# Kernel tuning notes

Hardware: AMD Instinct MI355X
Metric: run time of the kernel (lower is better)

Reference implementation:

```python
import jax, jax.numpy as jnp
import numpy as np

N = 50000   # total nodes across batched graphs
E = 800000  # total edges
F = 30      # input node features
G = 256     # number of graphs in the disjoint batch
CH = [128, 64, 32]
N_LABELS = 2


def setup_inputs() -> dict:
    key = jax.random.key(0)
    ks = jax.random.split(key, 16)
    x = jax.random.normal(ks[0], (N, F), dtype=jnp.float32)
    edge_weight = jax.random.uniform(ks[1], (E,), dtype=jnp.float32)
    edge_row = jax.random.randint(ks[2], (E,), 0, N, dtype=jnp.int32)
    edge_col = jax.random.randint(ks[3], (E,), 0, N, dtype=jnp.int32)
    seg = jnp.sort(jax.random.randint(ks[4], (N,), 0, G, dtype=jnp.int32))
    # GCSConv params: out = A @ (x W1) + x W2 + b, per layer
    dims = [F] + CH
    params = {}
    kk = 5
    for l in range(3):
        fin, fout = dims[l], dims[l + 1]
        s = 1.0 / np.sqrt(fin)
        params[f"w1_{l+1}"] = jax.random.uniform(ks[kk], (fin, fout), minval=-s, maxval=s, dtype=jnp.float32); kk += 1
        params[f"w2_{l+1}"] = jax.random.uniform(ks[kk], (fin, fout), minval=-s, maxval=s, dtype=jnp.float32); kk += 1
        params[f"b_{l+1}"] = jnp.zeros((fout,), dtype=jnp.float32)
    sd = 1.0 / np.sqrt(CH[-1])
    params["wd"] = jax.random.uniform(ks[kk], (CH[-1], N_LABELS), minval=-sd, maxval=sd, dtype=jnp.float32)
    params["bd"] = jnp.zeros((N_LABELS,), dtype=jnp.float32)
    return {"x": x, "edge_weight": edge_weight, "edge_row": edge_row,
            "edge_col": edge_col, "seg": seg, **params}


def _gcs_conv(x, ew, er, ec, w1, w2, b):
    # spektral GCSConv: relu(A @ (x W1) + x W2 + b) with sparse A in COO form
    h = x @ w1                                   # [N, Fout]
    msgs = ew[:, None] * h[ec]                   # gather along edges [E, Fout]
    agg = jax.ops.segment_sum(msgs, er, num_segments=N)  # SpMM scatter [N, Fout]
    return jax.nn.relu(agg + x @ w2 + b)


def reference(x, edge_weight, edge_row, edge_col, seg,
              w1_1, w2_1, b_1, w1_2, w2_2, b_2, w1_3, w2_3, b_3, wd, bd):
    h = _gcs_conv(x, edge_weight, edge_row, edge_col, w1_1, w2_1, b_1)
    h = _gcs_conv(h, edge_weight, edge_row, edge_col, w1_2, w2_2, b_2)
    h = _gcs_conv(h, edge_weight, edge_row, edge_col, w1_3, w2_3, b_3)
    # GlobalAvgPool: segment mean over graph ids
    sums = jax.ops.segment_sum(h, seg, num_segments=G)               # [G, 32]
    cnts = jax.ops.segment_sum(jnp.ones((N,), h.dtype), seg, num_segments=G)
    pooled = sums / jnp.maximum(cnts, 1.0)[:, None]
    return jax.nn.softmax(pooled @ wd + bd, axis=-1)                 # [G, 2]
```

## Files before the change

### kernel.cpp

```cpp
#include <hip/hip_runtime.h>
#include <hip/hip_fp16.h>

#define N_NODES 50000
#define N_EDGES 800000
#define N_GRAPHS 256
#define NCB 196
#define CHUNK 3125
#define MBLK 782

typedef _Float16 f16x8 __attribute__((ext_vector_type(8)));
typedef float    f32x4 __attribute__((ext_vector_type(4)));

__global__ __launch_bounds__(256)
void hist_prep(const int* __restrict__ ER, const float* __restrict__ X,
               const int* __restrict__ SEG,
               const float* __restrict__ W1, const float* __restrict__ W2,
               const float* __restrict__ W12, const float* __restrict__ W22,
               const float* __restrict__ W13, const float* __restrict__ W23,
               int* __restrict__ ghist, __half* __restrict__ XPh,
               int* __restrict__ start,
               __half* __restrict__ W1f, __half* __restrict__ W2f,
               __half* __restrict__ W3f, float* __restrict__ PS)
{
    int b = blockIdx.x;
    int t = threadIdx.x;
    if (b < 256) {
        __shared__ int h[NCB];
        for (int i = t; i < NCB; i += 256) h[i] = 0;
        __syncthreads();
        int lo = b * CHUNK, hi = lo + CHUNK;
        for (int e = lo + t; e < hi; e += 256) atomicAdd(&h[ER[e] >> 8], 1);
        __syncthreads();
        for (int i = t; i < NCB; i += 256) ghist[i * 256 + b] = h[i];
        return;
    }
    int bid = b - 256;
    if (bid < 6250) {
        int idx = bid * 256 + t;
        int n = idx >> 5;
        int c = idx & 31;
        float v = (c < 30) ? X[n * 30 + c] : 0.f;
        XPh[(size_t)n * 32 + c] = __float2half(v);
    } else if (bid < 6446) {
        int n = (bid - 6250) * 256 + t;
        if (n >= N_NODES) return;
        int g = SEG[n];
        int gprev = (n == 0) ? -1 : SEG[n - 1];
        for (int gg = gprev + 1; gg <= g; ++gg) start[gg] = n;
        if (n == N_NODES - 1)
            for (int gg = g + 1; gg <= N_GRAPHS; ++gg) start[gg] = N_NODES;
    } else if (bid < 6558) {
        int idx = (bid - 6446) * 256 + t;
        if (idx < 8192) {
            int i = idx & 7, c = (idx >> 3) & 15, g = (idx >> 7) & 3;
            int s = (idx >> 9) & 1, n = idx >> 10;
            int k = s * 32 + g * 8 + i, col = n * 16 + c;
            float w = 0.f;
            if (k < 30) w = W1[k * 128 + col];
            else if (k >= 32 && k < 62) w = W2[(k - 32) * 128 + col];
            W1f[idx] = __float2half(w);
        } else if (idx < 24576) {
            int o = idx - 8192;
            int i = o & 7, c = (o >> 3) & 15, g = (o >> 7) & 3;
            int s = (o >> 9) & 3, n = o >> 11;
            int k = s * 32 + g * 8 + i, col = n * 16 + c;
            float w = (col < 64) ? W12[k * 64 + col] : W22[k * 64 + col - 64];
            W2f[o] = __float2half(w);
        } else {
            int o = idx - 24576;
            int i = o & 7, c = (o >> 3) & 15, g = (o >> 7) & 3;
            int s = (o >> 9) & 1, n = o >> 10;
            int k = s * 32 + g * 8 + i, col = n * 16 + c;
            float w = (col < 32) ? W13[k * 32 + col] : W23[k * 32 + col - 32];
            W3f[o] = __float2half(w);
        }
    } else {
        int idx = (bid - 6558) * 256 + t;
        PS[idx] = 0.f;
    }
}

__global__ __launch_bounds__(256)
void scan1(int* __restrict__ ghist, int* __restrict__ bsum)
{
    __shared__ int s[256];
    int t = threadIdx.x, b = blockIdx.x;
    int i = b * 256 + t;
    int v = ghist[i];
    s[t] = v;
    __syncthreads();
    for (int off = 1; off < 256; off <<= 1) {
        int u = (t >= off) ? s[t - off] : 0;
        __syncthreads();
        s[t] += u;
        __syncthreads();
    }
    ghist[i] = s[t] - v;
    if (t == 255) bsum[b] = s[255];
}

__global__ __launch_bounds__(256)
void c_scatter(const int* __restrict__ ER, const int* __restrict__ EC,
               const float* __restrict__ EW, const int* __restrict__ ghist,
               const int* __restrict__ bsum, unsigned int* __restrict__ tmp_sd,
               __half* __restrict__ tmp_w)
{
    __shared__ int s[256];
    __shared__ int cur[NCB];
    int t = threadIdx.x, blk = blockIdx.x;
    int v = (t < NCB) ? bsum[t] : 0;
    s[t] = v;
    __syncthreads();
    for (int off = 1; off < 256; off <<= 1) {
        int u = (t >= off) ? s[t - off] : 0;
        __syncthreads();
        s[t] += u;
        __syncthreads();
    }
    if (t < NCB) cur[t] = (s[t] - v) + ghist[t * 256 + blk];
    __syncthreads();
    int lo = blk * CHUNK, hi = lo + CHUNK;
    for (int e = lo + t; e < hi; e += 256) {
        int d = ER[e];
        int pos = atomicAdd(&cur[d >> 8], 1);
        tmp_sd[pos] = (unsigned int)EC[e] | ((unsigned int)(d & 255) << 16);
        tmp_w[pos] = __float2half(EW[e]);
    }
}

__device__ __forceinline__ void fma8h(float4& a0, float4& a1, float w,
                                      const uint4& raw)
{
    const __half2* hp = (const __half2*)&raw;
    float2 f0 = __half22float2(hp[0]);
    float2 f1 = __half22float2(hp[1]);
    float2 f2 = __half22float2(hp[2]);
    float2 f3 = __half22float2(hp[3]);
    a0.x = fmaf(w, f0.x, a0.x); a0.y = fmaf(w, f0.y, a0.y);
    a0.z = fmaf(w, f1.x, a0.z); a0.w = fmaf(w, f1.y, a0.w);
    a1.x = fmaf(w, f2.x, a1.x); a1.y = fmaf(w, f2.y, a1.y);
    a1.z = fmaf(w, f3.x, a1.z); a1.w = fmaf(w, f3.y, a1.w);
}

__global__ __launch_bounds__(512)
void bsort_aggx(const unsigned int* __restrict__ tmp_sd, const __half* __restrict__ tmp_w,
                const int* __restrict__ bsum, const __half* __restrict__ XPh,
                unsigned int* __restrict__ packed, int* __restrict__ rowptr,
                __half* __restrict__ CIa)
{
    __shared__ int s[256];
    __shared__ int hist[256];
    __shared__ int cur[256];
    __shared__ int r0arr[257];
    int t = threadIdx.x, b = blockIdx.x;

    if (t < 256) s[t] = (t < NCB) ? bsum[t] : 0;
    __syncthreads();
    for (int off = 1; off < 256; off <<= 1) {
        int u = 0;
        if (t < 256 && t >= off) u = s[t - off];
        __syncthreads();
        if (t < 256) s[t] += u;
        __syncthreads();
    }
    int cntb = bsum[b];
    int base = s[b] - cntb;
    int end  = base + cntb;
    __syncthreads();

    if (t < 256) hist[t] = 0;
    __syncthreads();
    for (int j = base + t; j < end; j += 512)
        atomicAdd(&hist[(tmp_sd[j] >> 16) & 255], 1);
    __syncthreads();
    int hv = 0;
    if (t < 256) { hv = hist[t]; s[t] = hv; }
    __syncthreads();
    for (int off = 1; off < 256; off <<= 1) {
        int u = 0;
        if (t < 256 && t >= off) u = s[t - off];
        __syncthreads();
        if (t < 256) s[t] += u;
        __syncthreads();
    }
    if (t < 256) {
        int excl = s[t] - hv;
        int n = b * 256 + t;
        if (n < N_NODES) rowptr[n] = base + excl;
        if (b == NCB - 1 && t == 0) rowptr[N_NODES] = N_EDGES;
        r0arr[t] = base + excl;
        cur[t] = base + excl;
        if (t == 0) r0arr[256] = end;
    }
    __syncthreads();
    for (int j = base + t; j < end; j += 512) {
        unsigned int sd = tmp_sd[j];
        unsigned short hb = __half_as_ushort(tmp_w[j]);
        int pos = atomicAdd(&cur[(sd >> 16) & 255], 1);
        packed[pos] = (sd & 0xFFFF) | ((unsigned int)hb << 16);
    }
    __syncthreads();

    #pragma unroll
    for (int pass = 0; pass < 2; ++pass) {
        int local = pass * 128 + (t >> 2);
        int q = t & 3;
        int n = b * 256 + local;
        if (n < N_NODES) {
            int r0 = r0arr[local], r1 = r0arr[local + 1];
            float4 acc0 = make_float4(0.f, 0.f, 0.f, 0.f);
            float4 acc1 = make_float4(0.f, 0.f, 0.f, 0.f);
            int j = r0;
            for (; j + 3 < r1; j += 4) {
                unsigned int ra = packed[j],     rb = packed[j + 1];
                unsigned int rc = packed[j + 2], rd = packed[j + 3];
                uint4 rawa = *(const uint4*)(XPh + (size_t)(ra & 0xFFFF) * 32 + q * 8);
                uint4 rawb = *(const uint4*)(XPh + (size_t)(rb & 0xFFFF) * 32 + q * 8);
                uint4 rawc = *(const uint4*)(XPh + (size_t)(rc & 0xFFFF) * 32 + q * 8);
                uint4 rawd = *(const uint4*)(XPh + (size_t)(rd & 0xFFFF) * 32 + q * 8);
                float wa = __half2float(__ushort_as_half((unsigned short)(ra >> 16)));
                float wb = __half2float(__ushort_as_half((unsigned short)(rb >> 16)));
                float wc = __half2float(__ushort_as_half((unsigned short)(rc >> 16)));
                float wd = __half2float(__ushort_as_half((unsigned short)(rd >> 16)));
                fma8h(acc0, acc1, wa, rawa);
                fma8h(acc0, acc1, wb, rawb);
                fma8h(acc0, acc1, wc, rawc);
                fma8h(acc0, acc1, wd, rawd);
            }
            for (; j < r1; ++j) {
                unsigned int r = packed[j];
                uint4 raw = *(const uint4*)(XPh + (size_t)(r & 0xFFFF) * 32 + q * 8);
                float w = __half2float(__ushort_as_half((unsigned short)(r >> 16)));
                fma8h(acc0, acc1, w, raw);
            }
            __half2 hb2[4];
            hb2[0] = __float22half2_rn(make_float2(acc0.x, acc0.y));
            hb2[1] = __float22half2_rn(make_float2(acc0.z, acc0.w));
            hb2[2] = __float22half2_rn(make_float2(acc1.x, acc1.y));
            hb2[3] = __float22half2_rn(make_float2(acc1.z, acc1.w));
            *(uint4*)(CIa + (size_t)n * 32 + q * 8) = *(uint4*)&hb2[0];
        }
    }
}

__global__ __launch_bounds__(256)
void dense12_mfma(const __half* __restrict__ CIa, const __half* __restrict__ XPh,
                  const __half* __restrict__ W1f, const float* __restrict__ B1,
                  const __half* __restrict__ W2f, const float* __restrict__ B2,
                  __half* __restrict__ H2h, __half* __restrict__ A2h)
{
    __shared__ __align__(16) __half As[64 * 72];
    __shared__ __align__(16) __half Hs[64 * 136];
    const int tid = threadIdx.x;
    const int m0 = blockIdx.x * 64;
    const int lane = tid & 63;
    const int w  = tid >> 6;
    const int lr = lane & 15;
    const int lg = lane >> 4;

    for (int idx = tid; idx < 512; idx += 256) {
        int row = idx >> 3, c8 = idx & 7;
        int gm = m0 + row;
        uint4 v = make_uint4(0, 0, 0, 0);
        if (gm < N_NODES) {
            const __half* src = (c8 < 4) ? (CIa + (size_t)gm * 32 + c8 * 8)
                                         : (XPh + (size_t)gm * 32 + (c8 - 4) * 8);
            v = *(const uint4*)src;
        }
        *(uint4*)(As + row * 72 + c8 * 8) = v;
    }
    __syncthreads();

    f32x4 acc[4][2];
    #pragma unroll
    for (int m = 0; m < 4; ++m)
        #pragma unroll
        for (int j = 0; j < 2; ++j)
            acc[m][j] = (f32x4){0.f, 0.f, 0.f, 0.f};

    #pragma unroll
    for (int s = 0; s < 2; ++s) {
        f16x8 a[4];
        #pragma unroll
        for (int m = 0; m < 4; ++m)
            a[m] = *(const f16x8*)(As + (m * 16 + lr) * 72 + s * 32 + lg * 8);
        #pragma unroll
        for (int j = 0; j < 2; ++j) {
            const int n = 2 * w + j;
            f16x8 b = *(const f16x8*)(W1f + (((n * 2 + s) * 4 + lg) * 16 + lr) * 8);
            #pragma unroll
            for (int m = 0; m < 4; ++m)
                acc[m][j] = __builtin_amdgcn_mfma_f32_16x16x32_f16(a[m], b, acc[m][j], 0, 0, 0);
        }
    }

    #pragma unroll
    for (int j = 0; j < 2; ++j) {
        const int n = 2 * w + j;
        const float bias = B1[n * 16 + lr];
        #pragma unroll
        for (int m = 0; m < 4; ++m)
            #pragma unroll
            for (int r = 0; r < 4; ++r) {
                float v = fmaxf(acc[m][j][r] + bias, 0.f);
                Hs[(m * 16 + lg * 4 + r) * 136 + n * 16 + lr] = __float2half(v);
            }
    }
    __syncthreads();

    f32x4 acc2[4][2];
    #pragma unroll
    for (int m = 0; m < 4; ++m)
        #pragma unroll
        for (int j = 0; j < 2; ++j)
            acc2[m][j] = (f32x4){0.f, 0.f, 0.f, 0.f};

    #pragma unroll
    for (int s = 0; s < 4; ++s) {
        f16x8 a[4];
        #pragma unroll
        for (int m = 0; m < 4; ++m)
            a[m] = *(const f16x8*)(Hs + (m * 16 + lr) * 136 + s * 32 + lg * 8);
        #pragma unroll
        for (int j = 0; j < 2; ++j) {
            const int n = 2 * w + j;
            f16x8 b = *(const f16x8*)(W2f + (((n * 4 + s) * 4 + lg) * 16 + lr) * 8);
            #pragma unroll
            for (int m = 0; m < 4; ++m)
                acc2[m][j] = __builtin_amdgcn_mfma_f32_16x16x32_f16(a[m], b, acc2[m][j], 0, 0, 0);
        }
    }
    __syncthreads();

    #pragma unroll
    for (int j = 0; j < 2; ++j) {
        const int n = 2 * w + j;
        const float bias = (n >= 4) ? B2[(n - 4) * 16 + lr] : 0.f;
        #pragma unroll
        for (int m = 0; m < 4; ++m)
            #pragma unroll
            for (int r = 0; r < 4; ++r)
                Hs[(m * 16 + lg * 4 + r) * 136 + n * 16 + lr] =
                    __float2half(acc2[m][j][r] + bias);
    }
    __syncthreads();

    for (int idx = tid; idx < 1024; idx += 256) {
        int row = idx >> 4, c8 = idx & 15;
        int gm = m0 + row;
        if (gm < N_NODES) {
            uint4 v = *(const uint4*)(Hs + row * 136 + c8 * 8);
            if (c8 < 8) *(uint4*)(H2h + (size_t)gm * 64 + c8 * 8) = v;
            else        *(uint4*)(A2h + (size_t)gm * 64 + (c8 - 8) * 8) = v;
        }
    }
}

__global__ __launch_bounds__(512)
void spmm_dense3(const __half* __restrict__ H2h, const int* __restrict__ rowptr,
                 const unsigned int* __restrict__ packed,
                 const __half* __restrict__ A2h, const __half* __restrict__ W3f,
                 const float* __restrict__ B3, __half* __restrict__ H3h,
                 __half* __restrict__ B2h)
{
    __shared__ __align__(16) __half As[64 * 72];
    __shared__ __align__(16) __half Os[64 * 72];
    const int tid = threadIdx.x;
    const int m0 = blockIdx.x * 64;

    {
        int local = tid >> 3;
        int q = tid & 7;
        int n = m0 + local;
        float4 acc0 = make_float4(0.f, 0.f, 0.f, 0.f);
        float4 acc1 = make_float4(0.f, 0.f, 0.f, 0.f);
        if (n < N_NODES) {
            {
                uint4 raw = *(const uint4*)(A2h + (size_t)n * 64 + q * 8);
                const __half2* hp = (const __half2*)&raw;
                float2 f0 = __half22float2(hp[0]);
                float2 f1 = __half22float2(hp[1]);
                float2 f2 = __half22float2(hp[2]);
                float2 f3 = __half22float2(hp[3]);
                acc0 = make_float4(f0.x, f0.y, f1.x, f1.y);
                acc1 = make_float4(f2.x, f2.y, f3.x, f3.y);
            }
            int r0 = rowptr[n], r1 = rowptr[n + 1];
            int j = r0;
            for (; j + 3 < r1; j += 4) {
                unsigned int ra = packed[j],     rb = packed[j + 1];
                unsigned int rc = packed[j + 2], rd = packed[j + 3];
                uint4 rawa = *(const uint4*)(H2h + (size_t)(ra & 0xFFFF) * 64 + q * 8);
                uint4 rawb = *(const uint4*)(H2h + (size_t)(rb & 0xFFFF) * 64 + q * 8);
                uint4 rawc = *(const uint4*)(H2h + (size_t)(rc & 0xFFFF) * 64 + q * 8);
                uint4 rawd = *(const uint4*)(H2h + (size_t)(rd & 0xFFFF) * 64 + q * 8);
                float wa = __half2float(__ushort_as_half((unsigned short)(ra >> 16)));
                float wb = __half2float(__ushort_as_half((unsigned short)(rb >> 16)));
                float wc = __half2float(__ushort_as_half((unsigned short)(rc >> 16)));
                float wd = __half2float(__ushort_as_half((unsigned short)(rd >> 16)));
                fma8h(acc0, acc1, wa, rawa);
                fma8h(acc0, acc1, wb, rawb);
                fma8h(acc0, acc1, wc, rawc);
                fma8h(acc0, acc1, wd, rawd);
            }
            for (; j < r1; ++j) {
                unsigned int r = packed[j];
                uint4 raw = *(const uint4*)(H2h + (size_t)(r & 0xFFFF) * 64 + q * 8);
                float w = __half2float(__ushort_as_half((unsigned short)(r >> 16)));
                fma8h(acc0, acc1, w, raw);
            }
        }
        __half2 hb[4];
        hb[0] = __float22half2_rn(make_float2(fmaxf(acc0.x, 0.f), fmaxf(acc0.y, 0.f)));
        hb[1] = __float22half2_rn(make_float2(fmaxf(acc0.z, 0.f), fmaxf(acc0.w, 0.f)));
        hb[2] = __float22half2_rn(make_float2(fmaxf(acc1.x, 0.f), fmaxf(acc1.y, 0.f)));
        hb[3] = __float22half2_rn(make_float2(fmaxf(acc1.z, 0.f), fmaxf(acc1.w, 0.f)));
        *(uint4*)(As + local * 72 + q * 8) = *(uint4*)&hb[0];
    }
    __syncthreads();

    const int lane = tid & 63;
    const int w  = tid >> 6;
    const int wm = w >> 2;
    const int wn = w & 3;
    const int lr = lane & 15;
    const int lg = lane >> 4;

    f32x4 acc[2];
    acc[0] = (f32x4){0.f, 0.f, 0.f, 0.f};
    acc[1] = (f32x4){0.f, 0.f, 0.f, 0.f};

    #pragma unroll
    for (int s = 0; s < 2; ++s) {
        f16x8 b = *(const f16x8*)(W3f + (((wn * 2 + s) * 4 + lg) * 16 + lr) * 8);
        #pragma unroll
        for (int m = 0; m < 2; ++m) {
            int mm = wm * 2 + m;
            f16x8 a = *(const f16x8*)(As + (mm * 16 + lr) * 72 + s * 32 + lg * 8);
            acc[m] = __builtin_amdgcn_mfma_f32_16x16x32_f16(a, b, acc[m], 0, 0, 0);
        }
    }

    const float bias = (wn >= 2) ? B3[(wn - 2) * 16 + lr] : 0.f;
    #pragma unroll
    for (int m = 0; m < 2; ++m) {
        int mm = wm * 2 + m;
        #pragma unroll
        for (int r = 0; r < 4; ++r)
            Os[(mm * 16 + lg * 4 + r) * 72 + wn * 16 + lr] =
                __float2half(acc[m][r] + bias);
    }
    __syncthreads();

    {
        int row = tid >> 3, c8 = tid & 7;
        int gm = m0 + row;
        if (gm < N_NODES) {
            uint4 v = *(const uint4*)(Os + row * 72 + c8 * 8);
            if (c8 < 4) *(uint4*)(H3h + (size_t)gm * 32 + c8 * 8) = v;
            else        *(uint4*)(B2h + (size_t)gm * 32 + (c8 - 4) * 8) = v;
        }
    }
}

__global__ __launch_bounds__(256)
void spmm_pool(const __half* __restrict__ H, const int* __restrict__ rowptr,
               const unsigned int* __restrict__ packed,
               const __half* __restrict__ Bse, const int* __restrict__ SEG,
               float* __restrict__ PS)
{
    __shared__ float ps[65][32];
    int tid = threadIdx.x;
    int local = tid >> 2;
    int q = tid & 3;
    int n0 = blockIdx.x * 64;
    int n = n0 + local;
    for (int i = tid; i < 65 * 32; i += 256) ((float*)ps)[i] = 0.f;
    __syncthreads();
    int g0 = SEG[n0];
    if (n < N_NODES) {
        int g = SEG[n];
        int r0 = rowptr[n], r1 = rowptr[n + 1];
        float4 acc0, acc1;
        {
            uint4 raw = *(const uint4*)(Bse + (size_t)n * 32 + q * 8);
            const __half2* hp = (const __half2*)&raw;
            float2 f0 = __half22float2(hp[0]);
            float2 f1 = __half22float2(hp[1]);
            float2 f2 = __half22float2(hp[2]);
            float2 f3 = __half22float2(hp[3]);
            acc0 = make_float4(f0.x, f0.y, f1.x, f1.y);
            acc1 = make_float4(f2.x, f2.y, f3.x, f3.y);
        }
        int j = r0;
        for (; j + 3 < r1; j += 4) {
            unsigned int ra = packed[j],     rb = packed[j + 1];
            unsigned int rc = packed[j + 2], rd = packed[j + 3];
            uint4 rawa = *(const uint4*)(H + (size_t)(ra & 0xFFFF) * 32 + q * 8);
            uint4 rawb = *(const uint4*)(H + (size_t)(rb & 0xFFFF) * 32 + q * 8);
            uint4 rawc = *(const uint4*)(H + (size_t)(rc & 0xFFFF) * 32 + q * 8);
            uint4 rawd = *(const uint4*)(H + (size_t)(rd & 0xFFFF) * 32 + q * 8);
            float wa = __half2float(__ushort_as_half((unsigned short)(ra >> 16)));
            float wb = __half2float(__ushort_as_half((unsigned short)(rb >> 16)));
            float wc = __half2float(__ushort_as_half((unsigned short)(rc >> 16)));
            float wd = __half2float(__ushort_as_half((unsigned short)(rd >> 16)));
            fma8h(acc0, acc1, wa, rawa);
            fma8h(acc0, acc1, wb, rawb);
            fma8h(acc0, acc1, wc, rawc);
            fma8h(acc0, acc1, wd, rawd);
        }
        for (; j < r1; ++j) {
            unsigned int r = packed[j];
            uint4 raw = *(const uint4*)(H + (size_t)(r & 0xFFFF) * 32 + q * 8);
            float w = __half2float(__ushort_as_half((unsigned short)(r >> 16)));
            fma8h(acc0, acc1, w, raw);
        }
        float* dst = &ps[g - g0][q * 8];
        atomicAdd(&dst[0], fmaxf(acc0.x, 0.f));
        atomicAdd(&dst[1], fmaxf(acc0.y, 0.f));
        atomicAdd(&dst[2], fmaxf(acc0.z, 0.f));
        atomicAdd(&dst[3], fmaxf(acc0.w, 0.f));
        atomicAdd(&dst[4], fmaxf(acc1.x, 0.f));
        atomicAdd(&dst[5], fmaxf(acc1.y, 0.f));
        atomicAdd(&dst[6], fmaxf(acc1.z, 0.f));
        atomicAdd(&dst[7], fmaxf(acc1.w, 0.f));
    }
    __syncthreads();
    int nlast = n0 + 63;
    if (nlast >= N_NODES) nlast = N_NODES - 1;
    int span = SEG[nlast] - g0 + 1;
    for (int i = tid; i < span * 32; i += 256) {
        float v = ps[i >> 5][i & 31];
        if (v != 0.f)
            atomicAdd(&PS[(size_t)(g0 + (i >> 5)) * 32 + (i & 31)], v);
    }
}

__global__ __launch_bounds__(256)
void head_kernel(const float* __restrict__ PS, const int* __restrict__ start,
                 const float* __restrict__ WD, const float* __restrict__ BD,
                 float* __restrict__ OUT)
{
    int g = threadIdx.x;
    int s = start[g], e = start[g + 1];
    float inv = (e > s) ? 1.0f / (float)(e - s) : 1.0f;
    float l0 = 0.f, l1 = 0.f;
    #pragma unroll
    for (int j = 0; j < 32; ++j) {
        float p = PS[g * 32 + j] * inv;
        l0 = fmaf(p, WD[j * 2 + 0], l0);
        l1 = fmaf(p, WD[j * 2 + 1], l1);
    }
    l0 += BD[0]; l1 += BD[1];
    float m = fmaxf(l0, l1);
    float e0 = expf(l0 - m), e1 = expf(l1 - m);
    float si = 1.0f / (e0 + e1);
    OUT[g * 2 + 0] = e0 * si;
    OUT[g * 2 + 1] = e1 * si;
}

extern "C" void kernel_launch(void* const* d_in, const int* in_sizes, int n_in,
                              void* d_out, int out_size, void* d_ws, size_t ws_size,
                              hipStream_t stream)
{
    const float* x    = (const float*)d_in[0];
    const float* ew   = (const float*)d_in[1];
    const int*   er   = (const int*)d_in[2];
    const int*   ec   = (const int*)d_in[3];
    const int*   seg  = (const int*)d_in[4];
    const float* w1_1 = (const float*)d_in[5];
    const float* w2_1 = (const float*)d_in[6];
    const float* b_1  = (const float*)d_in[7];
    const float* w1_2 = (const float*)d_in[8];
    const float* w2_2 = (const float*)d_in[9];
    const float* b_2  = (const float*)d_in[10];
    const float* w1_3 = (const float*)d_in[11];
    const float* w2_3 = (const float*)d_in[12];
    const float* b_3  = (const float*)d_in[13];
    const float* wd   = (const float*)d_in[14];
    const float* bd   = (const float*)d_in[15];

    float* ws = (float*)d_ws;
    int*   IW = (int*)d_ws;
    __half* XPh    = (__half*)ws;
    __half* CIa    = (__half*)(ws + 800000);
    unsigned int* tmp_sd = (unsigned int*)(ws + 1600000);
    __half* tmp_w  = (__half*)(ws + 2400000);
    __half* H2h    = (__half*)(ws + 3200000);
    __half* A2h    = (__half*)(ws + 4800000);
    __half* H3h    = (__half*)(ws + 6400000);
    __half* B2h    = (__half*)(ws + 7200000);
    unsigned int* packed = (unsigned int*)(IW + 8000000);
    int*    rowptr = IW + 9000000;
    int*    ghist  = IW + 9060000;
    int*    bsum   = IW + 9115000;
    int*    start  = IW + 9120000;
    __half* W1f    = (__half*)(ws + 9125000);
    __half* W2f    = (__half*)(ws + 9130000);
    __half* W3f    = (__half*)(ws + 9139000);
    float*  PS     = ws + 9145000;

    dim3 blk(256);

    hist_prep<<<dim3(256 + 6590), blk, 0, stream>>>(er, x, seg, w1_1, w2_1,
                                                    w1_2, w2_2, w1_3, w2_3,
                                                    ghist, XPh, start,
                                                    W1f, W2f, W3f, PS);
    scan1<<<dim3(NCB), blk, 0, stream>>>(ghist, bsum);
    c_scatter<<<dim3(256), blk, 0, stream>>>(er, ec, ew, ghist, bsum, tmp_sd, tmp_w);
    bsort_aggx<<<dim3(NCB), dim3(512), 0, stream>>>(tmp_sd, tmp_w, bsum, XPh,
                                                    packed, rowptr, CIa);

    dense12_mfma<<<dim3(MBLK), blk, 0, stream>>>(CIa, XPh, W1f, b_1,
                                                 W2f, b_2, H2h, A2h);
    spmm_dense3<<<dim3(MBLK), dim3(512), 0, stream>>>(H2h, rowptr, packed, A2h,
                                                      W3f, b_3, H3h, B2h);
    spmm_pool<<<dim3(MBLK), blk, 0, stream>>>(H3h, rowptr, packed, B2h, seg, PS);
    head_kernel<<<dim3(1), blk, 0, stream>>>(PS, start, wd, bd, (float*)d_out);
}
```

Baseline: 182.4 us.

## Degree-sort nodes for SpMM load balancing across waves

Builds a global degree histogram and a permutation that orders nodes by in-degree, so the SpMM phases in spmm_dense3 and spmm_pool process rows of similar length together and warp divergence from uneven edge counts drops. bsort_aggx also reorders its local rows by degree. Because permuted rows no longer map to contiguous graphs, spmm_pool now keeps a full 256-graph shared accumulator and flushes all of it with global atomics. The cost is an extra kernel launch, gathers through the permutation that scatter the output writes, and a larger shared-memory pool with more atomic flushes.

```diff
diff --git a/kernel.cpp b/kernel.cpp
--- a/kernel.cpp
+++ b/kernel.cpp
@@ -20,7 +20,8 @@
                int* __restrict__ ghist, __half* __restrict__ XPh,
                int* __restrict__ start,
                __half* __restrict__ W1f, __half* __restrict__ W2f,
-               __half* __restrict__ W3f, float* __restrict__ PS)
+               __half* __restrict__ W3f, float* __restrict__ PS,
+               int* __restrict__ dhist, int* __restrict__ dcnt)
 {
     int b = blockIdx.x;
     int t = threadIdx.x;
@@ -76,7 +77,9 @@
         }
     } else {
         int idx = (bid - 6558) * 256 + t;
-        PS[idx] = 0.f;
+        if (idx < 8192) PS[idx] = 0.f;
+        else if (idx < 8256) dhist[idx - 8192] = 0;
+        else if (idx < 8320) dcnt[idx - 8256] = 0;
     }
 }
 
@@ -146,15 +149,19 @@
 void bsort_aggx(const unsigned int* __restrict__ tmp_sd, const __half* __restrict__ tmp_w,
                 const int* __restrict__ bsum, const __half* __restrict__ XPh,
                 unsigned int* __restrict__ packed, int* __restrict__ rowptr,
-                __half* __restrict__ CIa)
+                __half* __restrict__ CIa, int* __restrict__ dhist)
 {
     __shared__ int s[256];
     __shared__ int hist[256];
     __shared__ int cur[256];
     __shared__ int r0arr[257];
+    __shared__ int lh[64];
+    __shared__ int lbase[64];
+    __shared__ int lperm[256];
     int t = threadIdx.x, b = blockIdx.x;
 
     if (t < 256) s[t] = (t < NCB) ? bsum[t] : 0;
+    if (t >= 448) lh[t - 448] = 0;
     __syncthreads();
     for (int off = 1; off < 256; off <<= 1) {
         int u = 0;
@@ -183,6 +190,8 @@
         if (t < 256) s[t] += u;
         __syncthreads();
     }
+    int myd = 0, myrank = 0;
+    const int nvalid = (b * 256 + 256 <= N_NODES) ? 256 : (N_NODES - b * 256);
     if (t < 256) {
         int excl = s[t] - hv;
         int n = b * 256 + t;
@@ -191,8 +200,17 @@
         r0arr[t] = base + excl;
         cur[t] = base + excl;
         if (t == 0) r0arr[256] = end;
-    }
-    __syncthreads();
+        if (t < nvalid) {
+            myd = (hv < 63) ? hv : 63;
+            myrank = atomicAdd(&lh[myd], 1);
+        }
+    }
+    __syncthreads();
+    if (t < 64 && lh[t] > 0) atomicAdd(&dhist[t], lh[t]);
+    if (t == 511) {
+        int acc = 0;
+        for (int i = 0; i < 64; ++i) { lbase[i] = acc; acc += lh[i]; }
+    }
     for (int j = base + t; j < end; j += 512) {
         unsigned int sd = tmp_sd[j];
         unsigned short hb = __half_as_ushort(tmp_w[j]);
@@ -200,13 +218,16 @@
         packed[pos] = (sd & 0xFFFF) | ((unsigned int)hb << 16);
     }
     __syncthreads();
+    if (t < nvalid) lperm[lbase[myd] + myrank] = t;
+    __syncthreads();
 
     #pragma unroll
     for (int pass = 0; pass < 2; ++pass) {
-        int local = pass * 128 + (t >> 2);
+        int idx = pass * 128 + (t >> 2);
         int q = t & 3;
-        int n = b * 256 + local;
-        if (n < N_NODES) {
+        if (idx < nvalid) {
+            int local = lperm[idx];
+            int n = b * 256 + local;
             int r0 = r0arr[local], r1 = r0arr[local + 1];
             float4 acc0 = make_float4(0.f, 0.f, 0.f, 0.f);
             float4 acc1 = make_float4(0.f, 0.f, 0.f, 0.f);
@@ -244,6 +265,32 @@
 }
 
 __global__ __launch_bounds__(256)
+void perm_scatter(const int* __restrict__ rowptr, const int* __restrict__ dhist,
+                  int* __restrict__ dcnt, int* __restrict__ perm)
+{
+    __shared__ int lh[64], gbase[64], dbase[64];
+    int t = threadIdx.x, b = blockIdx.x;
+    int n = b * 256 + t;
+    if (t < 64) lh[t] = 0;
+    __syncthreads();
+    int d = 0, myr = 0;
+    bool valid = (n < N_NODES);
+    if (valid) {
+        d = rowptr[n + 1] - rowptr[n];
+        if (d > 63) d = 63;
+        myr = atomicAdd(&lh[d], 1);
+    }
+    __syncthreads();
+    if (t < 64) gbase[t] = (lh[t] > 0) ? atomicAdd(&dcnt[t], lh[t]) : 0;
+    if (t == 0) {
+        int acc = 0;
+        for (int i = 0; i < 64; ++i) { dbase[i] = acc; acc += dhist[i]; }
+    }
+    __syncthreads();
+    if (valid) perm[dbase[d] + gbase[d] + myr] = n;
+}
+
+__global__ __launch_bounds__(256)
 void dense12_mfma(const __half* __restrict__ CIa, const __half* __restrict__ XPh,
                   const __half* __restrict__ W1f, const float* __restrict__ B1,
                   const __half* __restrict__ W2f, const float* __restrict__ B2,
@@ -361,7 +408,7 @@
                  const unsigned int* __restrict__ packed,
                  const __half* __restrict__ A2h, const __half* __restrict__ W3f,
                  const float* __restrict__ B3, __half* __restrict__ H3h,
-                 __half* __restrict__ B2h)
+                 __half* __restrict__ B2h, const int* __restrict__ perm)
 {
     __shared__ __align__(16) __half As[64 * 72];
     __shared__ __align__(16) __half Os[64 * 72];
@@ -371,10 +418,11 @@
     {
         int local = tid >> 3;
         int q = tid & 7;
-        int n = m0 + local;
+        int i = m0 + local;
         float4 acc0 = make_float4(0.f, 0.f, 0.f, 0.f);
         float4 acc1 = make_float4(0.f, 0.f, 0.f, 0.f);
-        if (n < N_NODES) {
+        if (i < N_NODES) {
+            int n = perm[i];
             {
                 uint4 raw = *(const uint4*)(A2h + (size_t)n * 64 + q * 8);
                 const __half2* hp = (const __half2*)&raw;
@@ -454,8 +502,9 @@
 
     {
         int row = tid >> 3, c8 = tid & 7;
-        int gm = m0 + row;
-        if (gm < N_NODES) {
+        int i = m0 + row;
+        if (i < N_NODES) {
+            int gm = perm[i];
             uint4 v = *(const uint4*)(Os + row * 72 + c8 * 8);
             if (c8 < 4) *(uint4*)(H3h + (size_t)gm * 32 + c8 * 8) = v;
             else        *(uint4*)(B2h + (size_t)gm * 32 + (c8 - 4) * 8) = v;
@@ -467,18 +516,17 @@
 void spmm_pool(const __half* __restrict__ H, const int* __restrict__ rowptr,
                const unsigned int* __restrict__ packed,
                const __half* __restrict__ Bse, const int* __restrict__ SEG,
-               float* __restrict__ PS)
-{
-    __shared__ float ps[65][32];
+               float* __restrict__ PS, const int* __restrict__ perm)
+{
+    __shared__ float ps[N_GRAPHS][32];
     int tid = threadIdx.x;
     int local = tid >> 2;
     int q = tid & 3;
-    int n0 = blockIdx.x * 64;
-    int n = n0 + local;
-    for (int i = tid; i < 65 * 32; i += 256) ((float*)ps)[i] = 0.f;
-    __syncthreads();
-    int g0 = SEG[n0];
-    if (n < N_NODES) {
+    int i = blockIdx.x * 64 + local;
+    for (int k = tid; k < N_GRAPHS * 32; k += 256) ((float*)ps)[k] = 0.f;
+    __syncthreads();
+    if (i < N_NODES) {
+        int n = perm[i];
         int g = SEG[n];
         int r0 = rowptr[n], r1 = rowptr[n + 1];
         float4 acc0, acc1;
@@ -515,7 +563,7 @@
             float w = __half2float(__ushort_as_half((unsigned short)(r >> 16)));
             fma8h(acc0, acc1, w, raw);
         }
-        float* dst = &ps[g - g0][q * 8];
+        float* dst = &ps[g][q * 8];
         atomicAdd(&dst[0], fmaxf(acc0.x, 0.f));
         atomicAdd(&dst[1], fmaxf(acc0.y, 0.f));
         atomicAdd(&dst[2], fmaxf(acc0.z, 0.f));
@@ -526,13 +574,9 @@
         atomicAdd(&dst[7], fmaxf(acc1.w, 0.f));
     }
     __syncthreads();
-    int nlast = n0 + 63;
-    if (nlast >= N_NODES) nlast = N_NODES - 1;
-    int span = SEG[nlast] - g0 + 1;
-    for (int i = tid; i < span * 32; i += 256) {
-        float v = ps[i >> 5][i & 31];
-        if (v != 0.f)
-            atomicAdd(&PS[(size_t)(g0 + (i >> 5)) * 32 + (i & 31)], v);
+    for (int k = tid; k < N_GRAPHS * 32; k += 256) {
+        float v = ((float*)ps)[k];
+        if (v != 0.f) atomicAdd(&PS[k], v);
     }
 }
 
@@ -599,22 +643,27 @@
     __half* W2f    = (__half*)(ws + 9130000);
     __half* W3f    = (__half*)(ws + 9139000);
     float*  PS     = ws + 9145000;
+    int*    perm   = IW + 9155000;
+    int*    dhist  = IW + 9210000;
+    int*    dcnt   = IW + 9210064;
 
     dim3 blk(256);
 
-    hist_prep<<<dim3(256 + 6590), blk, 0, stream>>>(er, x, seg, w1_1, w2_1,
+    hist_prep<<<dim3(256 + 6591), blk, 0, stream>>>(er, x, seg, w1_1, w2_1,
                                                     w1_2, w2_2, w1_3, w2_3,
                                                     ghist, XPh, start,
-                                                    W1f, W2f, W3f, PS);
+                                                    W1f, W2f, W3f, PS,
+                                                    dhist, dcnt);
     scan1<<<dim3(NCB), blk, 0, stream>>>(ghist, bsum);
     c_scatter<<<dim3(256), blk, 0, stream>>>(er, ec, ew, ghist, bsum, tmp_sd, tmp_w);
     bsort_aggx<<<dim3(NCB), dim3(512), 0, stream>>>(tmp_sd, tmp_w, bsum, XPh,
-                                                    packed, rowptr, CIa);
+                                                    packed, rowptr, CIa, dhist);
+    perm_scatter<<<dim3(NCB), blk, 0, stream>>>(rowptr, dhist, dcnt, perm);
 
     dense12_mfma<<<dim3(MBLK), blk, 0, stream>>>(CIa, XPh, W1f, b_1,
                                                  W2f, b_2, H2h, A2h);
     spmm_dense3<<<dim3(MBLK), dim3(512), 0, stream>>>(H2h, rowptr, packed, A2h,
-                                                      W3f, b_3, H3h, B2h);
-    spmm_pool<<<dim3(MBLK), blk, 0, stream>>>(H3h, rowptr, packed, B2h, seg, PS);
+                                                      W3f, b_3, H3h, B2h, perm);
+    spmm_pool<<<dim3(MBLK), blk, 0, stream>>>(H3h, rowptr, packed, B2h, seg, PS, perm);
     head_kernel<<<dim3(1), blk, 0, stream>>>(PS, start, wd, bd, (float*)d_out);
 }
```

After: 188.8 us. 3.5% more time.

## Merge scan into scatter and fold head into pooling via last-block

Applied to the files above, without the earlier changes.

Removes the separate scan1 kernel by having each scatter block recompute per-bucket prefix and totals directly from the histogram. It also removes the single-block head kernel: the last block to finish pooling, found with an atomic counter, computes the mean, dense layer and softmax. This cuts two kernel launches and their inter-kernel gaps. In exchange every scatter block does redundant 256-wide row reads, and the head adds a fence plus an atomic counter reset in the prep kernel.

```diff
diff --git a/kernel.cpp b/kernel.cpp
--- a/kernel.cpp
+++ b/kernel.cpp
@@ -20,7 +20,8 @@
                int* __restrict__ ghist, __half* __restrict__ XPh,
                int* __restrict__ start,
                __half* __restrict__ W1f, __half* __restrict__ W2f,
-               __half* __restrict__ W3f, float* __restrict__ PS)
+               __half* __restrict__ W3f, float* __restrict__ PS,
+               int* __restrict__ done)
 {
     int b = blockIdx.x;
     int t = threadIdx.x;
@@ -76,40 +77,31 @@
         }
     } else {
         int idx = (bid - 6558) * 256 + t;
-        PS[idx] = 0.f;
+        if (idx < 8192) PS[idx] = 0.f;
+        else if (idx == 8192) *done = 0;
     }
 }
 
 __global__ __launch_bounds__(256)
-void scan1(int* __restrict__ ghist, int* __restrict__ bsum)
-{
-    __shared__ int s[256];
-    int t = threadIdx.x, b = blockIdx.x;
-    int i = b * 256 + t;
-    int v = ghist[i];
-    s[t] = v;
-    __syncthreads();
-    for (int off = 1; off < 256; off <<= 1) {
-        int u = (t >= off) ? s[t - off] : 0;
-        __syncthreads();
-        s[t] += u;
-        __syncthreads();
-    }
-    ghist[i] = s[t] - v;
-    if (t == 255) bsum[b] = s[255];
-}
-
-__global__ __launch_bounds__(256)
-void c_scatter(const int* __restrict__ ER, const int* __restrict__ EC,
-               const float* __restrict__ EW, const int* __restrict__ ghist,
-               const int* __restrict__ bsum, unsigned int* __restrict__ tmp_sd,
-               __half* __restrict__ tmp_w)
+void scan_scatter(const int* __restrict__ ER, const int* __restrict__ EC,
+                  const float* __restrict__ EW, const int* __restrict__ ghist,
+                  int* __restrict__ bsum, unsigned int* __restrict__ tmp_sd,
+                  __half* __restrict__ tmp_w)
 {
     __shared__ int s[256];
     __shared__ int cur[NCB];
     int t = threadIdx.x, blk = blockIdx.x;
-    int v = (t < NCB) ? bsum[t] : 0;
-    s[t] = v;
+    int partial = 0, total = 0;
+    if (t < NCB) {
+        const int* row = ghist + t * 256;
+        for (int b = 0; b < 256; ++b) {
+            int v = row[b];
+            partial += (b < blk) ? v : 0;
+            total += v;
+        }
+        if (blk == 0) bsum[t] = total;
+    }
+    s[t] = (t < NCB) ? total : 0;
     __syncthreads();
     for (int off = 1; off < 256; off <<= 1) {
         int u = (t >= off) ? s[t - off] : 0;
@@ -117,7 +109,7 @@
         s[t] += u;
         __syncthreads();
     }
-    if (t < NCB) cur[t] = (s[t] - v) + ghist[t * 256 + blk];
+    if (t < NCB) cur[t] = (s[t] - total) + partial;
     __syncthreads();
     int lo = blk * CHUNK, hi = lo + CHUNK;
     for (int e = lo + t; e < hi; e += 256) {
@@ -464,12 +456,15 @@
 }
 
 __global__ __launch_bounds__(256)
-void spmm_pool(const __half* __restrict__ H, const int* __restrict__ rowptr,
-               const unsigned int* __restrict__ packed,
-               const __half* __restrict__ Bse, const int* __restrict__ SEG,
-               float* __restrict__ PS)
+void spmm_pool_head(const __half* __restrict__ H, const int* __restrict__ rowptr,
+                    const unsigned int* __restrict__ packed,
+                    const __half* __restrict__ Bse, const int* __restrict__ SEG,
+                    float* __restrict__ PS, const int* __restrict__ start,
+                    const float* __restrict__ WD, const float* __restrict__ BD,
+                    int* __restrict__ done, float* __restrict__ OUT)
 {
     __shared__ float ps[65][32];
+    __shared__ int amLast;
     int tid = threadIdx.x;
     int local = tid >> 2;
     int q = tid & 3;
@@ -534,29 +529,29 @@
         if (v != 0.f)
             atomicAdd(&PS[(size_t)(g0 + (i >> 5)) * 32 + (i & 31)], v);
     }
-}
-
-__global__ __launch_bounds__(256)
-void head_kernel(const float* __restrict__ PS, const int* __restrict__ start,
-                 const float* __restrict__ WD, const float* __restrict__ BD,
-                 float* __restrict__ OUT)
-{
-    int g = threadIdx.x;
-    int s = start[g], e = start[g + 1];
-    float inv = (e > s) ? 1.0f / (float)(e - s) : 1.0f;
-    float l0 = 0.f, l1 = 0.f;
-    #pragma unroll
-    for (int j = 0; j < 32; ++j) {
-        float p = PS[g * 32 + j] * inv;
-        l0 = fmaf(p, WD[j * 2 + 0], l0);
-        l1 = fmaf(p, WD[j * 2 + 1], l1);
-    }
-    l0 += BD[0]; l1 += BD[1];
-    float m = fmaxf(l0, l1);
-    float e0 = expf(l0 - m), e1 = expf(l1 - m);
-    float si = 1.0f / (e0 + e1);
-    OUT[g * 2 + 0] = e0 * si;
-    OUT[g * 2 + 1] = e1 * si;
+    __threadfence();
+    __syncthreads();
+    if (tid == 0) amLast = (atomicAdd(done, 1) == (int)gridDim.x - 1);
+    __syncthreads();
+    if (amLast) {
+        __threadfence();
+        int g = tid;
+        int s = start[g], e = start[g + 1];
+        float inv = (e > s) ? 1.0f / (float)(e - s) : 1.0f;
+        float l0 = 0.f, l1 = 0.f;
+        #pragma unroll
+        for (int j = 0; j < 32; ++j) {
+            float p = atomicAdd(&PS[g * 32 + j], 0.f) * inv;
+            l0 = fmaf(p, WD[j * 2 + 0], l0);
+            l1 = fmaf(p, WD[j * 2 + 1], l1);
+        }
+        l0 += BD[0]; l1 += BD[1];
+        float m = fmaxf(l0, l1);
+        float e0 = expf(l0 - m), e1 = expf(l1 - m);
+        float si = 1.0f / (e0 + e1);
+        OUT[g * 2 + 0] = e0 * si;
+        OUT[g * 2 + 1] = e1 * si;
+    }
 }
 
 extern "C" void kernel_launch(void* const* d_in, const int* in_sizes, int n_in,
@@ -599,15 +594,16 @@
     __half* W2f    = (__half*)(ws + 9130000);
     __half* W3f    = (__half*)(ws + 9139000);
     float*  PS     = ws + 9145000;
+    int*    done   = IW + 9155000;
 
     dim3 blk(256);
 
-    hist_prep<<<dim3(256 + 6590), blk, 0, stream>>>(er, x, seg, w1_1, w2_1,
+    hist_prep<<<dim3(256 + 6591), blk, 0, stream>>>(er, x, seg, w1_1, w2_1,
                                                     w1_2, w2_2, w1_3, w2_3,
                                                     ghist, XPh, start,
-                                                    W1f, W2f, W3f, PS);
-    scan1<<<dim3(NCB), blk, 0, stream>>>(ghist, bsum);
-    c_scatter<<<dim3(256), blk, 0, stream>>>(er, ec, ew, ghist, bsum, tmp_sd, tmp_w);
+                                                    W1f, W2f, W3f, PS, done);
+    scan_scatter<<<dim3(256), blk, 0, stream>>>(er, ec, ew, ghist, bsum,
+                                                tmp_sd, tmp_w);
     bsort_aggx<<<dim3(NCB), dim3(512), 0, stream>>>(tmp_sd, tmp_w, bsum, XPh,
                                                     packed, rowptr, CIa);
 
@@ -615,6 +611,7 @@
                                                  W2f, b_2, H2h, A2h);
     spmm_dense3<<<dim3(MBLK), dim3(512), 0, stream>>>(H2h, rowptr, packed, A2h,
                                                       W3f, b_3, H3h, B2h);
-    spmm_pool<<<dim3(MBLK), blk, 0, stream>>>(H3h, rowptr, packed, B2h, seg, PS);
-    head_kernel<<<dim3(1), blk, 0, stream>>>(PS, start, wd, bd, (float*)d_out);
-}
+    spmm_pool_head<<<dim3(MBLK), blk, 0, stream>>>(H3h, rowptr, packed, B2h, seg,
+                                                   PS, start, wd, bd, done,
+                                                   (float*)d_out);
+}
```

Result: slower. 234.5 us (+28.6%).
